# Kernel optimization log

Hardware: AMD Instinct MI355X
Metric: run time of the kernel (lower is better)

## Reference

```python
import jax, jax.numpy as jnp
import numpy as np

B, P, L = 16, 196, 80
DIM1, DIM2, ATT = 2048, 300, 512
TAU = 1.0


def setup_inputs() -> dict:
    key = jax.random.key(0)
    ks = jax.random.split(key, 8)
    s1 = 1.0 / np.sqrt(DIM1)
    s2 = 1.0 / np.sqrt(DIM2)
    sa = 1.0 / np.sqrt(ATT)
    return {
        "x1": jax.random.normal(ks[0], (B, P, DIM1), dtype=jnp.float32),
        "x2": jax.random.normal(ks[1], (B, L, DIM2), dtype=jnp.float32),
        # nn.Linear weights stored as (out, in), like torch
        "W1": jax.random.uniform(ks[2], (ATT, DIM1), jnp.float32, -s1, s1),
        "W2": jax.random.uniform(ks[3], (ATT, DIM2), jnp.float32, -s2, s2),
        "Wh": jax.random.uniform(ks[4], (ATT, ATT), jnp.float32, -sa, sa),
        "bh": jax.random.uniform(ks[5], (ATT,), jnp.float32, -sa, sa),
        "Wt": jax.random.uniform(ks[6], (1, ATT), jnp.float32, -sa, sa),
        "bt": jax.random.uniform(ks[7], (1,), jnp.float32, -sa, sa),
    }


def reference(x1, x2, W1, W2, Wh, bh, Wt, bt):
    # projections: (B,P,ATT) and (B,L,ATT)
    p1 = jnp.einsum("bpd,ad->bpa", x1, W1)
    p2 = jnp.einsum("bld,ad->bla", x2, W2)
    # broadcast bilinear interaction: (B,L,P,ATT)
    m = jnp.tanh(p1[:, None, :, :] * p2[:, :, None, :])
    h = jnp.einsum("blpa,ca->blpc", m, Wh) + bh
    # score: (B,L,P)
    t = jnp.einsum("blpa,a->blp", h, Wt[0]) + bt[0]
    alpha = jax.nn.softmax(t / TAU, axis=-1)
    # weighted sum over pixels: (B,L,DIM1)
    label_repr = jnp.einsum("blp,bpd->bld", alpha, x1)
    return (label_repr, alpha)
```

## Files before the change

kernel.cpp:

```cpp
#include <hip/hip_runtime.h>

#define B_   16
#define P_   196
#define L_   80
#define DIM1 2048
#define DIM2 300
#define ATT  512

typedef __attribute__((ext_vector_type(8))) short short8x;
typedef __attribute__((ext_vector_type(8))) unsigned short ushort8x;
typedef __attribute__((ext_vector_type(4))) float f32x4;
typedef __attribute__((ext_vector_type(4))) unsigned int uint4x;
typedef __attribute__((ext_vector_type(4))) unsigned short ushort4x;

__device__ __forceinline__ unsigned short f2bf(float f) {
    unsigned v = __float_as_uint(f);
    v += 0x7fffu + ((v >> 16) & 1u);
    return (unsigned short)(v >> 16);
}

__global__ __launch_bounds__(256)
void prep_kernel(const float* __restrict__ x1, const float* __restrict__ W1,
                 const float* __restrict__ Wh, const float* __restrict__ Wt,
                 unsigned short* __restrict__ x1b, unsigned short* __restrict__ W1b,
                 float* __restrict__ w_eff) {
    __shared__ float part[4][64];
    const int blk = blockIdx.x, tid = threadIdx.x;
    if (blk < 2048) {
        const int n4 = (B_ * P_ * DIM1) / 4;
        for (int i = blk * 256 + tid; i < n4; i += 2048 * 256) {
            uint4x u = ((const uint4x*)x1)[i];
            ushort4x o;
            #pragma unroll
            for (int j = 0; j < 4; ++j) {
                unsigned v = u[j];
                v += 0x7fffu + ((v >> 16) & 1u);
                o[j] = (unsigned short)(v >> 16);
            }
            ((ushort4x*)x1b)[i] = o;
        }
    } else if (blk < 2560) {
        const int n4 = (ATT * DIM1) / 4;
        for (int i = (blk - 2048) * 256 + tid; i < n4; i += 512 * 256) {
            uint4x u = ((const uint4x*)W1)[i];
            ushort4x o;
            #pragma unroll
            for (int j = 0; j < 4; ++j) {
                unsigned v = u[j];
                v += 0x7fffu + ((v >> 16) & 1u);
                o[j] = (unsigned short)(v >> 16);
            }
            ((ushort4x*)W1b)[i] = o;
        }
    } else {
        const int bix = blk - 2560;
        const int lane = tid & 63, quad = tid >> 6;
        const int a = bix * 64 + lane;
        float s = 0.f;
        const int c0 = quad * 128;
        for (int c = c0; c < c0 + 128; ++c)
            s = fmaf(Wt[c], Wh[(size_t)c * ATT + a], s);
        part[quad][lane] = s;
        __syncthreads();
        if (tid < 64)
            w_eff[bix * 64 + tid] =
                (part[0][tid] + part[1][tid]) + (part[2][tid] + part[3][tid]);
    }
}

__global__ __launch_bounds__(256)
void gemm_nt(const float* __restrict__ A, const float* __restrict__ Bm,
             float* __restrict__ C, int M, int N, int K) {
    constexpr int BK = 16;
    __shared__ float As[BK][64];
    __shared__ float Bs[BK][64];
    const int tid  = threadIdx.x;
    const int bm   = blockIdx.x * 64;
    const int bn   = blockIdx.y * 64;
    const int ty   = tid >> 4;
    const int tx   = tid & 15;
    const int lrow = tid >> 2;
    const int lc4  = (tid & 3) << 2;
    float acc[4][4] = {};
    const float* Arow = A  + (size_t)(bm + lrow) * K;
    const float* Brow = Bm + (size_t)(bn + lrow) * K;

    for (int k0 = 0; k0 < K; k0 += BK) {
        float4 av, bv;
        if (k0 + BK <= K) {
            av = *(const float4*)(Arow + k0 + lc4);
            bv = *(const float4*)(Brow + k0 + lc4);
        } else {
            float a_[4], b_[4];
            #pragma unroll
            for (int i = 0; i < 4; ++i) {
                const int k = k0 + lc4 + i;
                a_[i] = (k < K) ? Arow[k] : 0.f;
                b_[i] = (k < K) ? Brow[k] : 0.f;
            }
            av = make_float4(a_[0], a_[1], a_[2], a_[3]);
            bv = make_float4(b_[0], b_[1], b_[2], b_[3]);
        }
        __syncthreads();
        As[lc4 + 0][lrow] = av.x;  As[lc4 + 1][lrow] = av.y;
        As[lc4 + 2][lrow] = av.z;  As[lc4 + 3][lrow] = av.w;
        Bs[lc4 + 0][lrow] = bv.x;  Bs[lc4 + 1][lrow] = bv.y;
        Bs[lc4 + 2][lrow] = bv.z;  Bs[lc4 + 3][lrow] = bv.w;
        __syncthreads();
        #pragma unroll
        for (int k = 0; k < BK; ++k) {
            const float4 a4 = *(const float4*)&As[k][ty << 2];
            const float4 b4 = *(const float4*)&Bs[k][tx << 2];
            const float ae[4] = {a4.x, a4.y, a4.z, a4.w};
            const float be[4] = {b4.x, b4.y, b4.z, b4.w};
            #pragma unroll
            for (int i = 0; i < 4; ++i)
                #pragma unroll
                for (int j = 0; j < 4; ++j)
                    acc[i][j] = fmaf(ae[i], be[j], acc[i][j]);
        }
    }
    #pragma unroll
    for (int i = 0; i < 4; ++i) {
        float4 o = make_float4(acc[i][0], acc[i][1], acc[i][2], acc[i][3]);
        *(float4*)(C + (size_t)(bm + (ty << 2) + i) * N + bn + (tx << 2)) = o;
    }
}

#define GM 3136
#define GN 512
#define GK 2048

__device__ __forceinline__ void gload16(const unsigned short* g, unsigned short* l) {
    __builtin_amdgcn_global_load_lds(
        (const __attribute__((address_space(1))) unsigned int*)g,
        (__attribute__((address_space(3))) unsigned int*)l, 16, 0, 0);
}

__global__ __launch_bounds__(256)
void gemm_bf16_mfma(const unsigned short* __restrict__ Ab,
                    const unsigned short* __restrict__ Bb,
                    unsigned short* __restrict__ C) {
    __shared__ unsigned short As[2][64 * 64];
    __shared__ unsigned short Bs[2][32 * 64];
    const int tid  = threadIdx.x;
    const int wid  = tid >> 6;
    const int lane = tid & 63;
    const int bm   = blockIdx.y * 64;
    const int bn   = blockIdx.x * 32;

    const int srow = lane >> 3;
    const int scol = ((lane & 7) ^ srow) << 3;
    const size_t arow0 = (size_t)(bm + (wid << 4) + srow) * GK;
    const size_t brow0 = (size_t)(bn + (wid << 3) + srow) * GK;

#define STAGE_TILE(buf, k0)                                                              \
    {                                                                                    \
        gload16(Ab + arow0 + (k0) + scol,                  &As[buf][((wid << 4) + 0) * 64]); \
        gload16(Ab + arow0 + (size_t)8 * GK + (k0) + scol, &As[buf][((wid << 4) + 8) * 64]); \
        gload16(Bb + brow0 + (k0) + scol,                  &Bs[buf][(wid << 3) * 64]);       \
    }

    f32x4 acc[2] = {};
    const int fr  = lane & 15;
    const int kb  = (lane >> 4) << 3;
    const int swz = (lane & 7) << 4;

    STAGE_TILE(0, 0)
    constexpr int NT = GK / 64;
    for (int kt = 0; kt < NT; ++kt) {
        __syncthreads();
        if (kt + 1 < NT) STAGE_TILE((kt + 1) & 1, (kt + 1) * 64)
        const char* pa = (const char*)&As[kt & 1][0];
        const char* pb = (const char*)&Bs[kt & 1][0];
        #pragma unroll
        for (int kk = 0; kk < 2; ++kk) {
            const int koff = ((kk * 32 + kb) * 2) ^ swz;
            short8x a = *(const short8x*)(pa + ((wid << 4) + fr) * 128 + koff);
            short8x b[2];
            #pragma unroll
            for (int n = 0; n < 2; ++n)
                b[n] = *(const short8x*)(pb + (n * 16 + fr) * 128 + koff);
            #pragma unroll
            for (int n = 0; n < 2; ++n)
                acc[n] = __builtin_amdgcn_mfma_f32_16x16x32_bf16(a, b[n], acc[n], 0, 0, 0);
        }
        __syncthreads();
    }

    const int crow = (lane >> 4) << 2;
    #pragma unroll
    for (int n = 0; n < 2; ++n)
        #pragma unroll
        for (int j = 0; j < 4; ++j)
            C[(size_t)(bm + (wid << 4) + crow + j) * GN + bn + n * 16 + fr] =
                f2bf(acc[n][j]);
#undef STAGE_TILE
}

#define LOG2E2 2.8853900817779268f

__global__ __launch_bounds__(256)
void score_softmax_kernel(const unsigned short* __restrict__ p1,
                          const float* __restrict__ p2,
                          const float* __restrict__ w_eff,
                          float* __restrict__ alpha) {
    const int bidx = blockIdx.x;
    const int bl = (bidx & 7) * 160 + (bidx >> 3);
    const int b  = bl / L_;
    __shared__ float s_t[P_];
    __shared__ float s_red[4];
    const int tid = threadIdx.x, wave = tid >> 6, lane = tid & 63;
    const int g = lane >> 4, c = lane & 15;

    const float4* gp2 = (const float4*)(p2 + (size_t)bl * ATT);
    const float4* gw  = (const float4*)w_eff;
    float qa[4][8], wa[4][8];
    #pragma unroll
    for (int j = 0; j < 4; ++j) {
        const float4 qlo = gp2[32 * j + 2 * c], qhi = gp2[32 * j + 2 * c + 1];
        const float4 wlo = gw[32 * j + 2 * c],  whi = gw[32 * j + 2 * c + 1];
        qa[j][0] = qlo.x * LOG2E2; qa[j][1] = qlo.y * LOG2E2;
        qa[j][2] = qlo.z * LOG2E2; qa[j][3] = qlo.w * LOG2E2;
        qa[j][4] = qhi.x * LOG2E2; qa[j][5] = qhi.y * LOG2E2;
        qa[j][6] = qhi.z * LOG2E2; qa[j][7] = qhi.w * LOG2E2;
        wa[j][0] = wlo.x; wa[j][1] = wlo.y; wa[j][2] = wlo.z; wa[j][3] = wlo.w;
        wa[j][4] = whi.x; wa[j][5] = whi.y; wa[j][6] = whi.z; wa[j][7] = whi.w;
    }

    const unsigned short* p1b = p1 + (size_t)b * P_ * ATT;
    const int nch = (wave == 0) ? 13 : 12;
    const int ptail = 192 + g;
    ushort8x cur[4], nxt[4];
    {
        const int row0 = 4 * wave + g;
        const ushort8x* row = (const ushort8x*)(p1b + (size_t)row0 * ATT);
        #pragma unroll
        for (int j = 0; j < 4; ++j) cur[j] = row[c + 16 * j];
    }
    for (int i = 0; i < nch; ++i) {
        const int pr = (i < 12) ? (16 * i + 4 * wave + g) : ptail;
        if (i + 1 < nch) {
            const int pn = (i + 1 < 12) ? (16 * (i + 1) + 4 * wave + g) : ptail;
            const ushort8x* row = (const ushort8x*)(p1b + (size_t)pn * ATT);
            #pragma unroll
            for (int j = 0; j < 4; ++j) nxt[j] = row[c + 16 * j];
        }
        float acc = 0.f;
        #pragma unroll
        for (int j = 0; j < 4; ++j) {
            float r[8];
            #pragma unroll
            for (int e = 0; e < 8; ++e)
                r[e] = __uint_as_float((unsigned)cur[j][e] << 16);
            #pragma unroll
            for (int pq = 0; pq < 4; ++pq) {
                const float e0 = __builtin_amdgcn_exp2f(r[2 * pq]     * qa[j][2 * pq]);
                const float e1 = __builtin_amdgcn_exp2f(r[2 * pq + 1] * qa[j][2 * pq + 1]);
                const float w0 = wa[j][2 * pq], w1 = wa[j][2 * pq + 1];
                const float num = fmaf(w0, e1, fmaf(w1, e0, w0 + w1));
                const float den = fmaf(e0, e1, e0 + e1 + 1.f);
                acc = fmaf(num, __builtin_amdgcn_rcpf(den), acc);
            }
        }
        acc += __shfl_xor(acc, 1);
        acc += __shfl_xor(acc, 2);
        acc += __shfl_xor(acc, 4);
        acc += __shfl_xor(acc, 8);
        if (c == 0) s_t[pr] = acc;
        #pragma unroll
        for (int j = 0; j < 4; ++j) cur[j] = nxt[j];
    }
    __syncthreads();
    const float v = (tid < P_) ? -2.f * s_t[tid] : -1e30f;
    float m = v;
    #pragma unroll
    for (int off = 32; off >= 1; off >>= 1) m = fmaxf(m, __shfl_xor(m, off));
    if (lane == 0) s_red[wave] = m;
    __syncthreads();
    m = fmaxf(fmaxf(s_red[0], s_red[1]), fmaxf(s_red[2], s_red[3]));
    __syncthreads();
    const float e = (tid < P_) ? __expf(v - m) : 0.f;
    float s = e;
    #pragma unroll
    for (int off = 32; off >= 1; off >>= 1) s += __shfl_xor(s, off);
    if (lane == 0) s_red[wave] = s;
    __syncthreads();
    s = s_red[0] + s_red[1] + s_red[2] + s_red[3];
    if (tid < P_) alpha[(size_t)bl * P_ + tid] = e / s;
}

__global__ __launch_bounds__(256)
void label_kernel(const float* __restrict__ alpha, const unsigned short* __restrict__ x1b,
                  float* __restrict__ out) {
    const int raw = blockIdx.x;
    const int dt = raw & 7;
    const int t  = raw >> 3;
    const int lt = t % 5;
    const int b  = t / 5;
    __shared__ float s_alpha[P_][16];
    const int tid = threadIdx.x;
    for (int idx = tid; idx < 16 * P_; idx += 256) {
        const int p = idx >> 4, i = idx & 15;
        s_alpha[p][i] = alpha[(size_t)(b * L_ + lt * 16 + i) * P_ + p];
    }
    __syncthreads();
    const int ty = tid >> 6, tx = tid & 63;
    const int d  = dt * 256 + tx * 4;
    const unsigned short* xp = x1b + (size_t)b * P_ * DIM1 + d;
    f32x4 acc[4] = {};
    for (int p = 0; p < P_; p += 4) {
        #pragma unroll
        for (int u = 0; u < 4; ++u) {
            const ushort4x xv = *(const ushort4x*)(xp + (size_t)(p + u) * DIM1);
            float xf[4];
            #pragma unroll
            for (int j = 0; j < 4; ++j)
                xf[j] = __uint_as_float((unsigned)xv[j] << 16);
            const float4 a = *(const float4*)&s_alpha[p + u][ty << 2];
            const float av[4] = {a.x, a.y, a.z, a.w};
            #pragma unroll
            for (int i2 = 0; i2 < 4; ++i2)
                #pragma unroll
                for (int j = 0; j < 4; ++j)
                    acc[i2][j] = fmaf(av[i2], xf[j], acc[i2][j]);
        }
    }
    const int lbase = b * L_ + lt * 16 + (ty << 2);
    #pragma unroll
    for (int i2 = 0; i2 < 4; ++i2)
        *(f32x4*)(out + (size_t)(lbase + i2) * DIM1 + d) = acc[i2];
}

extern "C" void kernel_launch(void* const* d_in, const int* in_sizes, int n_in,
                              void* d_out, int out_size, void* d_ws, size_t ws_size,
                              hipStream_t stream) {
    const float* x1 = (const float*)d_in[0];
    const float* x2 = (const float*)d_in[1];
    const float* W1 = (const float*)d_in[2];
    const float* W2 = (const float*)d_in[3];
    const float* Wh = (const float*)d_in[4];
    const float* Wt = (const float*)d_in[6];

    char* base = (char*)d_ws;
    unsigned short* p1b = (unsigned short*)base;
    float* p2    = (float*)(base + 3211264);
    float* w_eff = (float*)(base + 3211264 + 2621440);
    unsigned short* x1b = (unsigned short*)(base + 3211264 + 2621440 + 2048);
    unsigned short* W1b = x1b + (size_t)B_ * P_ * DIM1;

    float* label = (float*)d_out;
    float* alpha = label + (size_t)B_ * L_ * DIM1;

    hipLaunchKernelGGL(prep_kernel, dim3(2568), dim3(256), 0, stream,
                       x1, W1, Wh, Wt, x1b, W1b, w_eff);
    hipLaunchKernelGGL(gemm_nt, dim3((B_ * L_) / 64, ATT / 64), dim3(256), 0, stream,
                       x2, W2, p2, B_ * L_, ATT, DIM2);
    hipLaunchKernelGGL(gemm_bf16_mfma, dim3(GN / 32, GM / 64), dim3(256), 0, stream,
                       x1b, W1b, p1b);
    hipLaunchKernelGGL(score_softmax_kernel, dim3(B_ * L_), dim3(256), 0, stream,
                       p1b, p2, w_eff, alpha);
    hipLaunchKernelGGL(label_kernel, dim3(640), dim3(256), 0, stream,
                       alpha, x1b, label);
}
```

Baseline: 197.2 us.

## Fuse p2 GEMM into prep kernel, enlarge MFMA tile, drop softmax max pass

Folds the small x2·W2ᵀ fp32 GEMM into the prep kernel as extra blocks, saving one kernel launch. The bf16 MFMA GEMM tile grows from 64x32 to 64x64 with a 2x2 wave layout, which improves operand reuse but halves the block count. The softmax no longer subtracts the row maximum, which removes a reduction and barrier but risks overflow if scores get large. The score loop also precomputes paired weight sums.

```diff
diff --git a/kernel.cpp b/kernel.cpp
--- a/kernel.cpp
+++ b/kernel.cpp
@@ -22,13 +22,66 @@
 __global__ __launch_bounds__(256)
 void prep_kernel(const float* __restrict__ x1, const float* __restrict__ W1,
                  const float* __restrict__ Wh, const float* __restrict__ Wt,
+                 const float* __restrict__ x2, const float* __restrict__ W2,
                  unsigned short* __restrict__ x1b, unsigned short* __restrict__ W1b,
-                 float* __restrict__ w_eff) {
+                 float* __restrict__ w_eff, float* __restrict__ p2) {
+    __shared__ float As[16][64];
+    __shared__ float Bs[16][64];
     __shared__ float part[4][64];
     const int blk = blockIdx.x, tid = threadIdx.x;
-    if (blk < 2048) {
+
+    if (blk < 160) {
+        const int bm = (blk % 20) * 64;
+        const int bn = (blk / 20) * 64;
+        const int N = ATT, K = DIM2;
+        const int ty = tid >> 4, tx = tid & 15;
+        const int lrow = tid >> 2, lc4 = (tid & 3) << 2;
+        float acc[4][4] = {};
+        const float* Arow = x2 + (size_t)(bm + lrow) * K;
+        const float* Brow = W2 + (size_t)(bn + lrow) * K;
+        for (int k0 = 0; k0 < K; k0 += 16) {
+            float4 av, bv;
+            if (k0 + 16 <= K) {
+                av = *(const float4*)(Arow + k0 + lc4);
+                bv = *(const float4*)(Brow + k0 + lc4);
+            } else {
+                float a_[4], b_[4];
+                #pragma unroll
+                for (int i = 0; i < 4; ++i) {
+                    const int k = k0 + lc4 + i;
+                    a_[i] = (k < K) ? Arow[k] : 0.f;
+                    b_[i] = (k < K) ? Brow[k] : 0.f;
+                }
+                av = make_float4(a_[0], a_[1], a_[2], a_[3]);
+                bv = make_float4(b_[0], b_[1], b_[2], b_[3]);
+            }
+            __syncthreads();
+            As[lc4 + 0][lrow] = av.x;  As[lc4 + 1][lrow] = av.y;
+            As[lc4 + 2][lrow] = av.z;  As[lc4 + 3][lrow] = av.w;
+            Bs[lc4 + 0][lrow] = bv.x;  Bs[lc4 + 1][lrow] = bv.y;
+            Bs[lc4 + 2][lrow] = bv.z;  Bs[lc4 + 3][lrow] = bv.w;
+            __syncthreads();
+            #pragma unroll
+            for (int k = 0; k < 16; ++k) {
+                const float4 a4 = *(const float4*)&As[k][ty << 2];
+                const float4 b4 = *(const float4*)&Bs[k][tx << 2];
+                const float ae[4] = {a4.x, a4.y, a4.z, a4.w};
+                const float be[4] = {b4.x, b4.y, b4.z, b4.w};
+                #pragma unroll
+                for (int i = 0; i < 4; ++i)
+                    #pragma unroll
+                    for (int j = 0; j < 4; ++j)
+                        acc[i][j] = fmaf(ae[i], be[j], acc[i][j]);
+            }
+        }
+        #pragma unroll
+        for (int i = 0; i < 4; ++i) {
+            float4 o = make_float4(acc[i][0], acc[i][1], acc[i][2], acc[i][3]);
+            *(float4*)(p2 + (size_t)(bm + (ty << 2) + i) * N + bn + (tx << 2)) = o;
+        }
+    } else if (blk < 2208) {
         const int n4 = (B_ * P_ * DIM1) / 4;
-        for (int i = blk * 256 + tid; i < n4; i += 2048 * 256) {
+        for (int i = (blk - 160) * 256 + tid; i < n4; i += 2048 * 256) {
             uint4x u = ((const uint4x*)x1)[i];
             ushort4x o;
             #pragma unroll
@@ -39,9 +92,9 @@
             }
             ((ushort4x*)x1b)[i] = o;
         }
-    } else if (blk < 2560) {
+    } else if (blk < 2720) {
         const int n4 = (ATT * DIM1) / 4;
-        for (int i = (blk - 2048) * 256 + tid; i < n4; i += 512 * 256) {
+        for (int i = (blk - 2208) * 256 + tid; i < n4; i += 512 * 256) {
             uint4x u = ((const uint4x*)W1)[i];
             ushort4x o;
             #pragma unroll
@@ -53,7 +106,7 @@
             ((ushort4x*)W1b)[i] = o;
         }
     } else {
-        const int bix = blk - 2560;
+        const int bix = blk - 2720;
         const int lane = tid & 63, quad = tid >> 6;
         const int a = bix * 64 + lane;
         float s = 0.f;
@@ -68,65 +121,6 @@
     }
 }
 
-__global__ __launch_bounds__(256)
-void gemm_nt(const float* __restrict__ A, const float* __restrict__ Bm,
-             float* __restrict__ C, int M, int N, int K) {
-    constexpr int BK = 16;
-    __shared__ float As[BK][64];
-    __shared__ float Bs[BK][64];
-    const int tid  = threadIdx.x;
-    const int bm   = blockIdx.x * 64;
-    const int bn   = blockIdx.y * 64;
-    const int ty   = tid >> 4;
-    const int tx   = tid & 15;
-    const int lrow = tid >> 2;
-    const int lc4  = (tid & 3) << 2;
-    float acc[4][4] = {};
-    const float* Arow = A  + (size_t)(bm + lrow) * K;
-    const float* Brow = Bm + (size_t)(bn + lrow) * K;
-
-    for (int k0 = 0; k0 < K; k0 += BK) {
-        float4 av, bv;
-        if (k0 + BK <= K) {
-            av = *(const float4*)(Arow + k0 + lc4);
-            bv = *(const float4*)(Brow + k0 + lc4);
-        } else {
-            float a_[4], b_[4];
-            #pragma unroll
-            for (int i = 0; i < 4; ++i) {
-                const int k = k0 + lc4 + i;
-                a_[i] = (k < K) ? Arow[k] : 0.f;
-                b_[i] = (k < K) ? Brow[k] : 0.f;
-            }
-            av = make_float4(a_[0], a_[1], a_[2], a_[3]);
-            bv = make_float4(b_[0], b_[1], b_[2], b_[3]);
-        }
-        __syncthreads();
-        As[lc4 + 0][lrow] = av.x;  As[lc4 + 1][lrow] = av.y;
-        As[lc4 + 2][lrow] = av.z;  As[lc4 + 3][lrow] = av.w;
-        Bs[lc4 + 0][lrow] = bv.x;  Bs[lc4 + 1][lrow] = bv.y;
-        Bs[lc4 + 2][lrow] = bv.z;  Bs[lc4 + 3][lrow] = bv.w;
-        __syncthreads();
-        #pragma unroll
-        for (int k = 0; k < BK; ++k) {
-            const float4 a4 = *(const float4*)&As[k][ty << 2];
-            const float4 b4 = *(const float4*)&Bs[k][tx << 2];
-            const float ae[4] = {a4.x, a4.y, a4.z, a4.w};
-            const float be[4] = {b4.x, b4.y, b4.z, b4.w};
-            #pragma unroll
-            for (int i = 0; i < 4; ++i)
-                #pragma unroll
-                for (int j = 0; j < 4; ++j)
-                    acc[i][j] = fmaf(ae[i], be[j], acc[i][j]);
-        }
-    }
-    #pragma unroll
-    for (int i = 0; i < 4; ++i) {
-        float4 o = make_float4(acc[i][0], acc[i][1], acc[i][2], acc[i][3]);
-        *(float4*)(C + (size_t)(bm + (ty << 2) + i) * N + bn + (tx << 2)) = o;
-    }
-}
-
 #define GM 3136
 #define GN 512
 #define GK 2048
@@ -142,26 +136,29 @@
                     const unsigned short* __restrict__ Bb,
                     unsigned short* __restrict__ C) {
     __shared__ unsigned short As[2][64 * 64];
-    __shared__ unsigned short Bs[2][32 * 64];
+    __shared__ unsigned short Bs[2][64 * 64];
     const int tid  = threadIdx.x;
     const int wid  = tid >> 6;
     const int lane = tid & 63;
     const int bm   = blockIdx.y * 64;
-    const int bn   = blockIdx.x * 32;
+    const int bn   = blockIdx.x * 64;
+    const int wm   = wid >> 1;
+    const int wn   = wid & 1;
 
     const int srow = lane >> 3;
     const int scol = ((lane & 7) ^ srow) << 3;
     const size_t arow0 = (size_t)(bm + (wid << 4) + srow) * GK;
-    const size_t brow0 = (size_t)(bn + (wid << 3) + srow) * GK;
-
-#define STAGE_TILE(buf, k0)                                                              \
-    {                                                                                    \
-        gload16(Ab + arow0 + (k0) + scol,                  &As[buf][((wid << 4) + 0) * 64]); \
+    const size_t brow0 = (size_t)(bn + (wid << 4) + srow) * GK;
+
+#define STAGE_TILE(buf, k0)                                                        \
+    {                                                                              \
+        gload16(Ab + arow0 + (k0) + scol,            &As[buf][((wid << 4) + 0) * 64]); \
         gload16(Ab + arow0 + (size_t)8 * GK + (k0) + scol, &As[buf][((wid << 4) + 8) * 64]); \
-        gload16(Bb + brow0 + (k0) + scol,                  &Bs[buf][(wid << 3) * 64]);       \
-    }
-
-    f32x4 acc[2] = {};
+        gload16(Bb + brow0 + (k0) + scol,            &Bs[buf][((wid << 4) + 0) * 64]); \
+        gload16(Bb + brow0 + (size_t)8 * GK + (k0) + scol, &Bs[buf][((wid << 4) + 8) * 64]); \
+    }
+
+    f32x4 acc[2][2] = {};
     const int fr  = lane & 15;
     const int kb  = (lane >> 4) << 3;
     const int swz = (lane & 7) << 4;
@@ -176,25 +173,31 @@
         #pragma unroll
         for (int kk = 0; kk < 2; ++kk) {
             const int koff = ((kk * 32 + kb) * 2) ^ swz;
-            short8x a = *(const short8x*)(pa + ((wid << 4) + fr) * 128 + koff);
-            short8x b[2];
+            short8x a[2], b[2];
+            #pragma unroll
+            for (int m = 0; m < 2; ++m)
+                a[m] = *(const short8x*)(pa + (wm * 32 + m * 16 + fr) * 128 + koff);
             #pragma unroll
             for (int n = 0; n < 2; ++n)
-                b[n] = *(const short8x*)(pb + (n * 16 + fr) * 128 + koff);
-            #pragma unroll
-            for (int n = 0; n < 2; ++n)
-                acc[n] = __builtin_amdgcn_mfma_f32_16x16x32_bf16(a, b[n], acc[n], 0, 0, 0);
+                b[n] = *(const short8x*)(pb + (wn * 32 + n * 16 + fr) * 128 + koff);
+            #pragma unroll
+            for (int m = 0; m < 2; ++m)
+                #pragma unroll
+                for (int n = 0; n < 2; ++n)
+                    acc[m][n] = __builtin_amdgcn_mfma_f32_16x16x32_bf16(a[m], b[n], acc[m][n], 0, 0, 0);
         }
         __syncthreads();
     }
 
     const int crow = (lane >> 4) << 2;
     #pragma unroll
-    for (int n = 0; n < 2; ++n)
-        #pragma unroll
-        for (int j = 0; j < 4; ++j)
-            C[(size_t)(bm + (wid << 4) + crow + j) * GN + bn + n * 16 + fr] =
-                f2bf(acc[n][j]);
+    for (int m = 0; m < 2; ++m)
+        #pragma unroll
+        for (int n = 0; n < 2; ++n)
+            #pragma unroll
+            for (int j = 0; j < 4; ++j)
+                C[(size_t)(bm + wm * 32 + m * 16 + crow + j) * GN + bn + wn * 32 + n * 16 + fr] =
+                    f2bf(acc[m][n][j]);
 #undef STAGE_TILE
 }
 
@@ -215,7 +218,7 @@
 
     const float4* gp2 = (const float4*)(p2 + (size_t)bl * ATT);
     const float4* gw  = (const float4*)w_eff;
-    float qa[4][8], wa[4][8];
+    float qa[4][8], wa[4][8], ws[4][4];
     #pragma unroll
     for (int j = 0; j < 4; ++j) {
         const float4 qlo = gp2[32 * j + 2 * c], qhi = gp2[32 * j + 2 * c + 1];
@@ -226,6 +229,8 @@
         qa[j][6] = qhi.z * LOG2E2; qa[j][7] = qhi.w * LOG2E2;
         wa[j][0] = wlo.x; wa[j][1] = wlo.y; wa[j][2] = wlo.z; wa[j][3] = wlo.w;
         wa[j][4] = whi.x; wa[j][5] = whi.y; wa[j][6] = whi.z; wa[j][7] = whi.w;
+        ws[j][0] = wlo.x + wlo.y; ws[j][1] = wlo.z + wlo.w;
+        ws[j][2] = whi.x + whi.y; ws[j][3] = whi.z + whi.w;
     }
 
     const unsigned short* p1b = p1 + (size_t)b * P_ * ATT;
@@ -257,8 +262,8 @@
             for (int pq = 0; pq < 4; ++pq) {
                 const float e0 = __builtin_amdgcn_exp2f(r[2 * pq]     * qa[j][2 * pq]);
                 const float e1 = __builtin_amdgcn_exp2f(r[2 * pq + 1] * qa[j][2 * pq + 1]);
-                const float w0 = wa[j][2 * pq], w1 = wa[j][2 * pq + 1];
-                const float num = fmaf(w0, e1, fmaf(w1, e0, w0 + w1));
+                const float num = fmaf(wa[j][2 * pq], e1,
+                                  fmaf(wa[j][2 * pq + 1], e0, ws[j][pq]));
                 const float den = fmaf(e0, e1, e0 + e1 + 1.f);
                 acc = fmaf(num, __builtin_amdgcn_rcpf(den), acc);
             }
@@ -272,15 +277,7 @@
         for (int j = 0; j < 4; ++j) cur[j] = nxt[j];
     }
     __syncthreads();
-    const float v = (tid < P_) ? -2.f * s_t[tid] : -1e30f;
-    float m = v;
-    #pragma unroll
-    for (int off = 32; off >= 1; off >>= 1) m = fmaxf(m, __shfl_xor(m, off));
-    if (lane == 0) s_red[wave] = m;
-    __syncthreads();
-    m = fmaxf(fmaxf(s_red[0], s_red[1]), fmaxf(s_red[2], s_red[3]));
-    __syncthreads();
-    const float e = (tid < P_) ? __expf(v - m) : 0.f;
+    const float e = (tid < P_) ? __builtin_amdgcn_exp2f(-LOG2E2 * s_t[tid]) : 0.f;
     float s = e;
     #pragma unroll
     for (int off = 32; off >= 1; off >>= 1) s += __shfl_xor(s, off);
@@ -352,11 +349,9 @@
     float* label = (float*)d_out;
     float* alpha = label + (size_t)B_ * L_ * DIM1;
 
-    hipLaunchKernelGGL(prep_kernel, dim3(2568), dim3(256), 0, stream,
-                       x1, W1, Wh, Wt, x1b, W1b, w_eff);
-    hipLaunchKernelGGL(gemm_nt, dim3((B_ * L_) / 64, ATT / 64), dim3(256), 0, stream,
-                       x2, W2, p2, B_ * L_, ATT, DIM2);
-    hipLaunchKernelGGL(gemm_bf16_mfma, dim3(GN / 32, GM / 64), dim3(256), 0, stream,
+    hipLaunchKernelGGL(prep_kernel, dim3(2728), dim3(256), 0, stream,
+                       x1, W1, Wh, Wt, x2, W2, x1b, W1b, w_eff, p2);
+    hipLaunchKernelGGL(gemm_bf16_mfma, dim3(GN / 64, GM / 64), dim3(256), 0, stream,
                        x1b, W1b, p1b);
     hipLaunchKernelGGL(score_softmax_kernel, dim3(B_ * L_), dim3(256), 0, stream,
                        p1b, p2, w_eff, alpha);
```

After: 187.5 us. 1.05x faster.
